# Optimization experiments

Measured on AMD Instinct MI355X. Metric: run time of the kernel, lower is better.

## Reference

```python
import jax, jax.numpy as jnp
import numpy as np

N_NODES = 100000
N_EDGES = 1600000
N_GRAPHS = 128
IN_FEATS = 128
OUT_FEATS = 64


def setup_inputs() -> dict:
    key = jax.random.key(0)
    k1, k2, k3, k4, k5, k6 = jax.random.split(key, 6)
    features = jax.random.normal(k1, (N_NODES, IN_FEATS), jnp.float32)
    src = jax.random.randint(k2, (N_EDGES,), 0, N_NODES, dtype=jnp.int32)
    dst = jax.random.randint(k3, (N_EDGES,), 0, N_NODES, dtype=jnp.int32)
    graph_ids = jnp.sort(jax.random.randint(k4, (N_NODES,), 0, N_GRAPHS, dtype=jnp.int32))
    # Xavier-uniform init as in DGL GraphConv
    lim1 = float(np.sqrt(6.0 / (IN_FEATS + IN_FEATS)))
    lim2 = float(np.sqrt(6.0 / (IN_FEATS + OUT_FEATS)))
    W1 = jax.random.uniform(k5, (IN_FEATS, IN_FEATS), jnp.float32, -lim1, lim1)
    W2 = jax.random.uniform(k6, (IN_FEATS, OUT_FEATS), jnp.float32, -lim2, lim2)
    b1 = jnp.zeros((IN_FEATS,), jnp.float32)
    b2 = jnp.zeros((OUT_FEATS,), jnp.float32)
    return {"features": features, "W1": W1, "b1": b1, "W2": W2, "b2": b2,
            "src": src, "dst": dst, "graph_ids": graph_ids, "num_graphs": N_GRAPHS}


def _graph_conv(x, W, b, src, dst, n_nodes):
    # DGL GraphConv, norm='both': D_dst^{-1/2} A D_src^{-1/2} X W + b
    ones = jnp.ones(src.shape, x.dtype)
    deg_out = jax.ops.segment_sum(ones, src, num_segments=n_nodes)
    deg_in = jax.ops.segment_sum(ones, dst, num_segments=n_nodes)
    norm_src = jax.lax.rsqrt(jnp.maximum(deg_out, 1.0))  # [N]
    norm_dst = jax.lax.rsqrt(jnp.maximum(deg_in, 1.0))   # [N]
    h = (x * norm_src[:, None]) @ W                       # dense transform first
    agg = jax.ops.segment_sum(h[src], dst, num_segments=n_nodes)  # spmm-style scatter-add
    return agg * norm_dst[:, None] + b


def reference(features, W1, b1, W2, b2, src, dst, graph_ids, num_graphs):
    n = features.shape[0]
    h = jax.nn.relu(_graph_conv(features, W1, b1, src, dst, n))
    h = jax.nn.relu(_graph_conv(h, W2, b2, src, dst, n))
    # dgl.mean_nodes: per-graph mean over nodes
    sums = jax.ops.segment_sum(h, graph_ids, num_segments=num_graphs)
    counts = jax.ops.segment_sum(jnp.ones((n, 1), h.dtype), graph_ids, num_segments=num_graphs)
    return sums / jnp.maximum(counts, 1.0)
```

## Files before the change

### kernel.cpp

```cpp
#include <hip/hip_runtime.h>
#include <hip/hip_bf16.h>


#define NPP_SHIFT 9
#define NPP 512
#define MAXP 256
#define NB 512
#define CAPP 10240

typedef __attribute__((ext_vector_type(8))) short frag8;
typedef __attribute__((ext_vector_type(4))) float f32x4;
typedef __attribute__((ext_vector_type(2))) float v2f;

__launch_bounds__(256)
__global__ void buildAC(const int* __restrict__ src, const int* __restrict__ dst,
                        int E, int P, int* __restrict__ cur,
                        int* __restrict__ ebuf_src, int2* __restrict__ ebuf_dst,
                        const int* __restrict__ gids, int N, int G,
                        int* __restrict__ gcnt) {
    __shared__ int hs[MAXP], hd[MAXP], bs1[MAXP], bs2[MAXP], hg[MAXP];
    int tid = threadIdx.x;
    for (int i = tid; i < MAXP; i += 256) { hs[i] = 0; hd[i] = 0; hg[i] = 0; }
    __syncthreads();
    int per_block = (E + NB - 1) / NB;
    int e0 = blockIdx.x * per_block;
    int e1 = min(e0 + per_block, E);
    for (int e = e0 + tid; e < e1; e += 256) {
        atomicAdd(&hs[src[e] >> NPP_SHIFT], 1);
        atomicAdd(&hd[dst[e] >> NPP_SHIFT], 1);
    }
    int npb = (N + NB - 1) / NB;
    int n0 = blockIdx.x * npb;
    int n1 = min(n0 + npb, N);
    for (int i = n0 + tid; i < n1; i += 256) atomicAdd(&hg[gids[i]], 1);
    __syncthreads();
    for (int p = tid; p < P; p += 256) {
        int c1 = hs[p];
        bs1[p] = c1 ? atomicAdd(&cur[p], c1) : 0;
        int c2 = hd[p];
        bs2[p] = c2 ? atomicAdd(&cur[P + p], c2) : 0;
        hs[p] = 0;
        hd[p] = 0;
    }
    for (int i = tid; i < G; i += 256)
        if (hg[i]) atomicAdd(&gcnt[i], hg[i]);
    __syncthreads();
    for (int e = e0 + tid; e < e1; e += 256) {
        int s = src[e];
        int d = dst[e];
        int p1 = s >> NPP_SHIFT;
        int p2 = d >> NPP_SHIFT;
        int l1 = atomicAdd(&hs[p1], 1);
        ebuf_src[(size_t)p1 * CAPP + bs1[p1] + l1] = s;
        int l2 = atomicAdd(&hd[p2], 1);
        ebuf_dst[(size_t)p2 * CAPP + bs2[p2] + l2] = make_int2(d, s);
    }
}

__launch_bounds__(512)
__global__ void passD3(const int* __restrict__ ebuf_src, const int2* __restrict__ ebuf_dst,
                       const int* __restrict__ cur, float* __restrict__ norm_src,
                       int* __restrict__ row_start, int* __restrict__ csr_src,
                       int N, int E, int P) {
    __shared__ int hs[NPP], hd[NPP], sc[NPP];
    int tid = threadIdx.x;
    int p = blockIdx.x;
    sc[tid] = (tid < P) ? cur[P + tid] : 0;
    __syncthreads();
    for (int off = 1; off < 512; off <<= 1) {
        int t = (tid >= off) ? sc[tid - off] : 0;
        __syncthreads();
        sc[tid] += t;
        __syncthreads();
    }
    int gbase = (p > 0) ? sc[p - 1] : 0;
    __syncthreads();
    int node_lo = p << NPP_SHIFT;
    int nl = min(NPP, N - node_lo);
    hs[tid] = 0;
    hd[tid] = 0;
    __syncthreads();
    int nsrc = cur[p];
    size_t base_s = (size_t)p * CAPP;
    for (int i = tid; i < nsrc; i += 512)
        atomicAdd(&hs[ebuf_src[base_s + i] - node_lo], 1);
    int ndst = cur[P + p];
    size_t base_d = (size_t)p * CAPP;
    for (int i = tid; i < ndst; i += 512)
        atomicAdd(&hd[ebuf_dst[base_d + i].x - node_lo], 1);
    __syncthreads();
    if (tid < nl) norm_src[node_lo + tid] = rsqrtf((float)max(hs[tid], 1));
    int myh = hd[tid];
    sc[tid] = myh;
    __syncthreads();
    for (int off = 1; off < 512; off <<= 1) {
        int t = (tid >= off) ? sc[tid - off] : 0;
        __syncthreads();
        sc[tid] += t;
        __syncthreads();
    }
    int row0 = gbase + sc[tid] - myh;
    if (tid < nl) row_start[node_lo + tid] = row0;
    if (p == P - 1 && tid == 0) row_start[N] = E;
    __syncthreads();
    hd[tid] = row0;
    __syncthreads();
    for (int i = tid; i < ndst; i += 512) {
        int2 r = ebuf_dst[base_d + i];
        int pos = atomicAdd(&hd[r.x - node_lo], 1);
        csr_src[pos] = r.y;
    }
}

template <int COLS, bool BF16IN, bool PERM, bool FP8OUT>
__launch_bounds__(256)
__global__ void gemm_mfma(const void* __restrict__ xin, const float* __restrict__ w,
                          const float* __restrict__ norm,
                          void* __restrict__ out, int n) {
    constexpr int NT = COLS / 16;
    __shared__ short wlds[4 * NT * 64 * 8];
    const int tid = threadIdx.x;
    for (int i = tid; i < 128 * COLS / 4; i += 256) {
        int k = (i * 4) / COLS;
        int n0 = (i * 4) % COLS;
        float4 wv;
        if constexpr (PERM) {
            int ksrc = 64 * ((k >> 2) & 1) + 16 * (k & 3) + (k >> 3);
            wv = *reinterpret_cast<const float4*>(w + (size_t)ksrc * COLS + n0);
        } else {
            wv = reinterpret_cast<const float4*>(w)[i];
        }
        int c = k >> 5, q = (k >> 3) & 3, j = k & 7;
        float vals[4] = {wv.x, wv.y, wv.z, wv.w};
#pragma unroll
        for (int u = 0; u < 4; ++u) {
            int nn = n0 + u;
            int t = nn >> 4;
            int ln = (q << 4) | (nn & 15);
            union { __hip_bfloat16 b; short s; } cv;
            cv.b = __float2bfloat16(vals[u]);
            wlds[(((c * NT + t) << 6) | ln) * 8 + j] = cv.s;
        }
    }
    __syncthreads();

    const int lane = tid & 63;
    const int wid = tid >> 6;
    const int m = lane & 15;
    const int q = lane >> 4;
    const int ntiles = (n + 15) >> 4;
    const frag8* wfr = reinterpret_cast<const frag8*>(wlds);

    for (int wt = blockIdx.x * 4 + wid; wt < ntiles; wt += gridDim.x * 4) {
        const int row = (wt << 4) + m;
        frag8 af[4];
        if (row < n) {
            if constexpr (BF16IN) {
                const frag8* xp = reinterpret_cast<const frag8*>(
                    (const __hip_bfloat16*)xin + (size_t)row * 128);
#pragma unroll
                for (int c = 0; c < 4; ++c) af[c] = xp[c * 4 + q];
            } else {
                const float* xp = (const float*)xin + (size_t)row * 128;
                float nm = norm[row];
#pragma unroll
                for (int c = 0; c < 4; ++c) {
                    int base = c * 32 + q * 8;
                    float4 v0 = *reinterpret_cast<const float4*>(xp + base);
                    float4 v1 = *reinterpret_cast<const float4*>(xp + base + 4);
                    union { frag8 f; short s[8]; } a;
                    union { __hip_bfloat16 b; short s; } cv;
                    cv.b = __float2bfloat16(v0.x * nm); a.s[0] = cv.s;
                    cv.b = __float2bfloat16(v0.y * nm); a.s[1] = cv.s;
                    cv.b = __float2bfloat16(v0.z * nm); a.s[2] = cv.s;
                    cv.b = __float2bfloat16(v0.w * nm); a.s[3] = cv.s;
                    cv.b = __float2bfloat16(v1.x * nm); a.s[4] = cv.s;
                    cv.b = __float2bfloat16(v1.y * nm); a.s[5] = cv.s;
                    cv.b = __float2bfloat16(v1.z * nm); a.s[6] = cv.s;
                    cv.b = __float2bfloat16(v1.w * nm); a.s[7] = cv.s;
                    af[c] = a.f;
                }
            }
        } else {
#pragma unroll
            for (int c = 0; c < 4; ++c) af[c] = frag8{0, 0, 0, 0, 0, 0, 0, 0};
        }
        f32x4 acc[NT] = {};
#pragma unroll
        for (int c = 0; c < 4; ++c)
#pragma unroll
            for (int t = 0; t < NT; ++t)
                acc[t] = __builtin_amdgcn_mfma_f32_16x16x32_bf16(
                    af[c], wfr[(c * NT + t) * 64 + lane], acc[t], 0, 0, 0);
#pragma unroll
        for (int r = 0; r < 4; ++r) {
            int grow = (wt << 4) + q * 4 + r;
            if (grow < n) {
                if constexpr (FP8OUT && COLS == 128) {
                    uint w0 = 0, w1 = 0;
                    w0 = (uint)__builtin_amdgcn_cvt_pk_fp8_f32(acc[0][r], acc[1][r], (int)w0, false);
                    w0 = (uint)__builtin_amdgcn_cvt_pk_fp8_f32(acc[2][r], acc[3][r], (int)w0, true);
                    w1 = (uint)__builtin_amdgcn_cvt_pk_fp8_f32(acc[4][r], acc[5][r], (int)w1, false);
                    w1 = (uint)__builtin_amdgcn_cvt_pk_fp8_f32(acc[6][r], acc[7][r], (int)w1, true);
                    reinterpret_cast<uint2*>(out)[(size_t)grow * 16 + m] = make_uint2(w0, w1);
                } else if constexpr (FP8OUT) {
                    uint w0 = 0;
                    w0 = (uint)__builtin_amdgcn_cvt_pk_fp8_f32(acc[0][r], acc[1][r], (int)w0, false);
                    w0 = (uint)__builtin_amdgcn_cvt_pk_fp8_f32(acc[2][r], acc[3][r], (int)w0, true);
                    reinterpret_cast<uint*>(out)[(size_t)grow * 16 + m] = w0;
                } else {
                    __hip_bfloat16* ob = reinterpret_cast<__hip_bfloat16*>(out);
#pragma unroll
                    for (int t = 0; t < NT; ++t)
                        ob[(size_t)grow * COLS + t * 16 + m] = __float2bfloat16(acc[t][r]);
                }
            }
        }
    }
}

__launch_bounds__(256)
__global__ void spmm1_kernel(const uint2* __restrict__ h1,
                             const int* __restrict__ row_start,
                             const int* __restrict__ csr_src,
                             const float* __restrict__ b1,
                             const float* __restrict__ norm_src,
                             uint4* __restrict__ x2n, int n) {
    int wv = (blockIdx.x * blockDim.x + threadIdx.x) >> 6;
    int lane = threadIdx.x & 63;
    int r0 = wv * 2;
    if (r0 >= n) return;
    int a = lane >> 4;
    int s = lane & 15;
    int e0[2], e1[2];
#pragma unroll
    for (int r = 0; r < 2; ++r) {
        int rr = min(r0 + r, n - 1);
        e0[r] = row_start[rr];
        e1[r] = row_start[rr + 1];
        if (r0 + r >= n) e1[r] = e0[r];
    }
    v2f acc[2][4] = {};
    int nb = max((e1[0] - e0[0] + 15) >> 4, (e1[1] - e0[1] + 15) >> 4);
    for (int b = 0; b < nb; ++b) {
        uint2 v[2][4];
#pragma unroll
        for (int r = 0; r < 2; ++r) {
            int base = e0[r] + b * 16;
            if (base + 16 <= e1[r]) {
#pragma unroll
                for (int j = 0; j < 4; ++j)
                    v[r][j] = h1[(size_t)csr_src[base + 4 * j + a] * 16 + s];
            } else if (base < e1[r]) {
#pragma unroll
                for (int j = 0; j < 4; ++j) {
                    int idx = base + 4 * j + a;
                    int cidx = min(idx, e1[r] - 1);
                    uint2 vv = h1[(size_t)csr_src[cidx] * 16 + s];
                    bool ok = idx < e1[r];
                    v[r][j].x = ok ? vv.x : 0u;
                    v[r][j].y = ok ? vv.y : 0u;
                }
            } else {
#pragma unroll
                for (int j = 0; j < 4; ++j) v[r][j] = make_uint2(0u, 0u);
            }
        }
#pragma unroll
        for (int r = 0; r < 2; ++r)
#pragma unroll
            for (int j = 0; j < 4; ++j) {
                acc[r][0] += __builtin_amdgcn_cvt_pk_f32_fp8((int)v[r][j].x, false);
                acc[r][1] += __builtin_amdgcn_cvt_pk_f32_fp8((int)v[r][j].x, true);
                acc[r][2] += __builtin_amdgcn_cvt_pk_f32_fp8((int)v[r][j].y, false);
                acc[r][3] += __builtin_amdgcn_cvt_pk_f32_fp8((int)v[r][j].y, true);
            }
    }
#pragma unroll
    for (int r = 0; r < 2; ++r)
#pragma unroll
        for (int k = 0; k < 4; ++k) {
            v2f t;
            t[0] = __shfl_xor(acc[r][k][0], 16);
            t[1] = __shfl_xor(acc[r][k][1], 16);
            acc[r][k] += t;
            t[0] = __shfl_xor(acc[r][k][0], 32);
            t[1] = __shfl_xor(acc[r][k][1], 32);
            acc[r][k] += t;
        }
    if (a == 0) {
        float bbl[4] = {b1[s], b1[32 + s], b1[64 + s], b1[96 + s]};
        float bbh[4] = {b1[16 + s], b1[48 + s], b1[80 + s], b1[112 + s]};
#pragma unroll
        for (int r = 0; r < 2; ++r) {
            if (r0 + r < n) {
                float nd = rsqrtf((float)max(e1[r] - e0[r], 1));
                float ns = norm_src[r0 + r];
                uint w[4];
#pragma unroll
                for (int k = 0; k < 4; ++k) {
                    float fl = fmaxf(fmaf(acc[r][k][0], nd, bbl[k]), 0.f) * ns;
                    float fh = fmaxf(fmaf(acc[r][k][1], nd, bbh[k]), 0.f) * ns;
                    union { __hip_bfloat16 b; ushort u; } cl, ch;
                    cl.b = __float2bfloat16(fl);
                    ch.b = __float2bfloat16(fh);
                    w[k] = (uint)cl.u | ((uint)ch.u << 16);
                }
                x2n[(size_t)(r0 + r) * 16 + s] = make_uint4(w[0], w[1], w[2], w[3]);
            }
        }
    }
}

__launch_bounds__(256)
__global__ void spmm2_kernel(const uint* __restrict__ h2,
                             const int* __restrict__ row_start,
                             const int* __restrict__ csr_src,
                             const float* __restrict__ b2,
                             const int* __restrict__ gids,
                             const int* __restrict__ gcnt,
                             float* __restrict__ out, int n) {
    int wv = (blockIdx.x * blockDim.x + threadIdx.x) >> 6;
    int lane = threadIdx.x & 63;
    int wave = threadIdx.x >> 6;
    int r0 = wv * 4;
    int a = lane >> 4;
    int s = lane & 15;
    int e0[4], e1[4], g[4];
    float inv[4];
#pragma unroll
    for (int r = 0; r < 4; ++r) {
        int rr = min(r0 + r, n - 1);
        e0[r] = row_start[rr];
        e1[r] = row_start[rr + 1];
        g[r] = gids[rr];
        if (r0 + r >= n) { e1[r] = e0[r]; g[r] = -1; }
        inv[r] = 1.f / (float)max(gcnt[max(g[r], 0)], 1);
    }
    float acc[4][4] = {};
    int nb = 0;
#pragma unroll
    for (int r = 0; r < 4; ++r) nb = max(nb, (e1[r] - e0[r] + 15) >> 4);
    for (int b = 0; b < nb; ++b) {
        uint u[4][4];
#pragma unroll
        for (int r = 0; r < 4; ++r) {
            int base = e0[r] + b * 16;
            if (base + 16 <= e1[r]) {
#pragma unroll
                for (int j = 0; j < 4; ++j)
                    u[r][j] = h2[(size_t)csr_src[base + 4 * j + a] * 16 + s];
            } else if (base < e1[r]) {
#pragma unroll
                for (int j = 0; j < 4; ++j) {
                    int idx = base + 4 * j + a;
                    int cidx = min(idx, e1[r] - 1);
                    uint vv = h2[(size_t)csr_src[cidx] * 16 + s];
                    u[r][j] = (idx < e1[r]) ? vv : 0u;
                }
            } else {
#pragma unroll
                for (int j = 0; j < 4; ++j) u[r][j] = 0u;
            }
        }
#pragma unroll
        for (int r = 0; r < 4; ++r)
#pragma unroll
            for (int j = 0; j < 4; ++j) {
                v2f lo = __builtin_amdgcn_cvt_pk_f32_fp8((int)u[r][j], false);
                v2f hi = __builtin_amdgcn_cvt_pk_f32_fp8((int)u[r][j], true);
                acc[r][0] += lo[0]; acc[r][1] += lo[1];
                acc[r][2] += hi[0]; acc[r][3] += hi[1];
            }
    }
#pragma unroll
    for (int r = 0; r < 4; ++r)
#pragma unroll
        for (int k = 0; k < 4; ++k) {
            acc[r][k] += __shfl_xor(acc[r][k], 16);
            acc[r][k] += __shfl_xor(acc[r][k], 32);
        }
    float bb0 = b2[s], bb1 = b2[16 + s], bb2v = b2[32 + s], bb3 = b2[48 + s];
    float val[4][4];
#pragma unroll
    for (int r = 0; r < 4; ++r) {
        float nd = rsqrtf((float)max(e1[r] - e0[r], 1));
        bool vld = g[r] >= 0;
        val[r][0] = vld ? fmaxf(fmaf(acc[r][0], nd, bb0), 0.f) * inv[r] : 0.f;
        val[r][1] = vld ? fmaxf(fmaf(acc[r][1], nd, bb1), 0.f) * inv[r] : 0.f;
        val[r][2] = vld ? fmaxf(fmaf(acc[r][2], nd, bb2v), 0.f) * inv[r] : 0.f;
        val[r][3] = vld ? fmaxf(fmaf(acc[r][3], nd, bb3), 0.f) * inv[r] : 0.f;
    }
    __shared__ float sbuf[4][64];
    __shared__ int sg[4];
    bool same = (g[0] == g[1]) && (g[1] == g[2]) && (g[2] == g[3]) && (g[0] >= 0);
    int sgw;
    if (same) {
        if (a == 0) {
            sbuf[wave][s]      = val[0][0] + val[1][0] + val[2][0] + val[3][0];
            sbuf[wave][16 + s] = val[0][1] + val[1][1] + val[2][1] + val[3][1];
            sbuf[wave][32 + s] = val[0][2] + val[1][2] + val[2][2] + val[3][2];
            sbuf[wave][48 + s] = val[0][3] + val[1][3] + val[2][3] + val[3][3];
        }
        sgw = g[0];
    } else {
        if (a == 0) {
#pragma unroll
            for (int r = 0; r < 4; ++r) {
                if (g[r] >= 0) {
                    atomicAdd(&out[(size_t)g[r] * 64 + s], val[r][0]);
                    atomicAdd(&out[(size_t)g[r] * 64 + 16 + s], val[r][1]);
                    atomicAdd(&out[(size_t)g[r] * 64 + 32 + s], val[r][2]);
                    atomicAdd(&out[(size_t)g[r] * 64 + 48 + s], val[r][3]);
                }
            }
            sbuf[wave][s] = 0.f;
            sbuf[wave][16 + s] = 0.f;
            sbuf[wave][32 + s] = 0.f;
            sbuf[wave][48 + s] = 0.f;
        }
        sgw = -1;
    }
    if (lane == 0) sg[wave] = sgw;
    __syncthreads();
    if (wave == 0) {
        int g0 = sg[0], g1 = sg[1], g2 = sg[2], g3 = sg[3];
        if (g0 == g1 && g1 == g2 && g2 == g3 && g0 >= 0) {
            float ssum = sbuf[0][lane] + sbuf[1][lane] + sbuf[2][lane] + sbuf[3][lane];
            atomicAdd(&out[(size_t)g0 * 64 + lane], ssum);
        } else {
#pragma unroll
            for (int w = 0; w < 4; ++w)
                if (sg[w] >= 0)
                    atomicAdd(&out[(size_t)sg[w] * 64 + lane], sbuf[w][lane]);
        }
    }
}

extern "C" void kernel_launch(void* const* d_in, const int* in_sizes, int n_in,
                              void* d_out, int out_size, void* d_ws, size_t ws_size,
                              hipStream_t stream) {
    const float* features = (const float*)d_in[0];
    const float* W1 = (const float*)d_in[1];
    const float* b1 = (const float*)d_in[2];
    const float* W2 = (const float*)d_in[3];
    const float* b2 = (const float*)d_in[4];
    const int* src = (const int*)d_in[5];
    const int* dst = (const int*)d_in[6];
    const int* gids = (const int*)d_in[7];
    const int N = in_sizes[7];
    const int E = in_sizes[5];
    const int G = out_size / 64;
    float* out = (float*)d_out;
    const int P = (N + NPP - 1) >> NPP_SHIFT;

    char* ws = (char*)d_ws;
    size_t off = 0;
    auto alloc = [&](size_t bytes) -> void* {
        void* p = ws + off;
        off = (off + bytes + 255) & ~(size_t)255;
        return p;
    };
    int* zblock = (int*)alloc((size_t)(G + 2 * P) * 4);
    int* gcnt = zblock;
    int* cur = zblock + G;
    int* ebuf_src = (int*)alloc((size_t)P * CAPP * 4);
    int2* ebuf_dst = (int2*)alloc((size_t)P * CAPP * 8);
    float* norm_src = (float*)alloc((size_t)N * 4);
    int* row_start = (int*)alloc((size_t)(N + 1) * 4);
    int* csr_src = (int*)alloc((size_t)E * 4);
    uint* h1 = (uint*)alloc((size_t)N * 128);
    __hip_bfloat16* x2n = (__hip_bfloat16*)alloc((size_t)N * 128 * 2);
    uint* h2 = h1;

    hipMemsetAsync(out, 0, (size_t)out_size * sizeof(float), stream);
    hipMemsetAsync(zblock, 0, (size_t)(G + 2 * P) * 4, stream);

    buildAC<<<NB, 256, 0, stream>>>(src, dst, E, P, cur, ebuf_src, ebuf_dst,
                                    gids, N, G, gcnt);
    passD3<<<P, 512, 0, stream>>>(ebuf_src, ebuf_dst, cur, norm_src, row_start,
                                  csr_src, N, E, P);

    gemm_mfma<128, false, false, true><<<768, 256, 0, stream>>>(features, W1, norm_src,
                                                                (void*)h1, N);
    {
        int waves = (N + 1) / 2;
        int blocks = (waves * 64 + 255) / 256;
        spmm1_kernel<<<blocks, 256, 0, stream>>>((const uint2*)h1, row_start, csr_src, b1,
                                                 norm_src, (uint4*)x2n, N);
    }
    gemm_mfma<64, true, true, true><<<768, 256, 0, stream>>>(x2n, W2, nullptr,
                                                             (void*)h2, N);
    {
        int waves = (N + 3) / 4;
        int blocks = (waves * 64 + 255) / 256;
        spmm2_kernel<<<blocks, 256, 0, stream>>>(h2, row_start, csr_src, b2,
                                                 gids, gcnt, out, N);
    }
}
```

Baseline: 285.0 us.

## Bucket edges via striped global atomics with packed compact edge buffers

```diff
diff --git a/kernel.cpp b/kernel.cpp
--- a/kernel.cpp
+++ b/kernel.cpp
@@ -6,109 +6,113 @@
 #define NPP 512
 #define MAXP 256
 #define NB 512
-#define CAPP 10240
+#define CAPB 1280
 
 typedef __attribute__((ext_vector_type(8))) short frag8;
 typedef __attribute__((ext_vector_type(4))) float f32x4;
 typedef __attribute__((ext_vector_type(2))) float v2f;
 
 __launch_bounds__(256)
-__global__ void buildAC(const int* __restrict__ src, const int* __restrict__ dst,
-                        int E, int P, int* __restrict__ cur,
-                        int* __restrict__ ebuf_src, int2* __restrict__ ebuf_dst,
-                        const int* __restrict__ gids, int N, int G,
-                        int* __restrict__ gcnt) {
-    __shared__ int hs[MAXP], hd[MAXP], bs1[MAXP], bs2[MAXP], hg[MAXP];
+__global__ void buildG(const int* __restrict__ src, const int* __restrict__ dst,
+                       int E, int P, int* __restrict__ cur,
+                       ushort* __restrict__ ebuf_src, uint* __restrict__ ebuf_dst,
+                       const int* __restrict__ gids, int N, int G,
+                       int* __restrict__ gcnt) {
+    __shared__ int hg[MAXP];
     int tid = threadIdx.x;
-    for (int i = tid; i < MAXP; i += 256) { hs[i] = 0; hd[i] = 0; hg[i] = 0; }
-    __syncthreads();
-    int per_block = (E + NB - 1) / NB;
-    int e0 = blockIdx.x * per_block;
-    int e1 = min(e0 + per_block, E);
-    for (int e = e0 + tid; e < e1; e += 256) {
-        atomicAdd(&hs[src[e] >> NPP_SHIFT], 1);
-        atomicAdd(&hd[dst[e] >> NPP_SHIFT], 1);
+    for (int i = tid; i < MAXP; i += 256) hg[i] = 0;
+    __syncthreads();
+    int stripe = blockIdx.x & 7;
+    int gt = blockIdx.x * 256 + tid;
+    int stride = gridDim.x * 256;
+    for (int e = gt; e < E; e += stride) {
+        int s = src[e];
+        int d = dst[e];
+        int p1 = s >> NPP_SHIFT;
+        int p2 = d >> NPP_SHIFT;
+        int pos1 = atomicAdd(&cur[(p1 << 3) | stripe], 1);
+        ebuf_src[(size_t)((p1 << 3) | stripe) * CAPB + pos1] = (ushort)(s & 511);
+        int pos2 = atomicAdd(&cur[P * 8 + ((p2 << 3) | stripe)], 1);
+        ebuf_dst[(size_t)((p2 << 3) | stripe) * CAPB + pos2] =
+            ((uint)(d & 511) << 17) | (uint)s;
     }
     int npb = (N + NB - 1) / NB;
     int n0 = blockIdx.x * npb;
     int n1 = min(n0 + npb, N);
     for (int i = n0 + tid; i < n1; i += 256) atomicAdd(&hg[gids[i]], 1);
     __syncthreads();
-    for (int p = tid; p < P; p += 256) {
-        int c1 = hs[p];
-        bs1[p] = c1 ? atomicAdd(&cur[p], c1) : 0;
-        int c2 = hd[p];
-        bs2[p] = c2 ? atomicAdd(&cur[P + p], c2) : 0;
-        hs[p] = 0;
-        hd[p] = 0;
-    }
     for (int i = tid; i < G; i += 256)
         if (hg[i]) atomicAdd(&gcnt[i], hg[i]);
-    __syncthreads();
-    for (int e = e0 + tid; e < e1; e += 256) {
-        int s = src[e];
-        int d = dst[e];
-        int p1 = s >> NPP_SHIFT;
-        int p2 = d >> NPP_SHIFT;
-        int l1 = atomicAdd(&hs[p1], 1);
-        ebuf_src[(size_t)p1 * CAPP + bs1[p1] + l1] = s;
-        int l2 = atomicAdd(&hd[p2], 1);
-        ebuf_dst[(size_t)p2 * CAPP + bs2[p2] + l2] = make_int2(d, s);
-    }
 }
 
-__launch_bounds__(512)
-__global__ void passD3(const int* __restrict__ ebuf_src, const int2* __restrict__ ebuf_dst,
+__launch_bounds__(1024)
+__global__ void passD4(const ushort* __restrict__ ebuf_src, const uint* __restrict__ ebuf_dst,
                        const int* __restrict__ cur, float* __restrict__ norm_src,
                        int* __restrict__ row_start, int* __restrict__ csr_src,
                        int N, int E, int P) {
     __shared__ int hs[NPP], hd[NPP], sc[NPP];
     int tid = threadIdx.x;
     int p = blockIdx.x;
-    sc[tid] = (tid < P) ? cur[P + tid] : 0;
+    if (tid < NPP) {
+        int tot = 0;
+        if (tid < P) {
+#pragma unroll
+            for (int t = 0; t < 8; ++t) tot += cur[P * 8 + (tid << 3) + t];
+        }
+        sc[tid] = tot;
+    }
     __syncthreads();
     for (int off = 1; off < 512; off <<= 1) {
-        int t = (tid >= off) ? sc[tid - off] : 0;
+        int t = (tid >= off && tid < 512) ? sc[tid - off] : 0;
         __syncthreads();
-        sc[tid] += t;
+        if (tid < 512) sc[tid] += t;
         __syncthreads();
     }
     int gbase = (p > 0) ? sc[p - 1] : 0;
+    __syncthreads();
+    if (tid < NPP) { hs[tid] = 0; hd[tid] = 0; }
+    __syncthreads();
+#pragma unroll
+    for (int t = 0; t < 8; ++t) {
+        int cnt = cur[(p << 3) + t];
+        const ushort* eb = ebuf_src + (size_t)((p << 3) + t) * CAPB;
+        for (int i = tid; i < cnt; i += 1024) atomicAdd(&hs[eb[i]], 1);
+    }
+#pragma unroll
+    for (int t = 0; t < 8; ++t) {
+        int cnt = cur[P * 8 + (p << 3) + t];
+        const uint* eb = ebuf_dst + (size_t)((p << 3) + t) * CAPB;
+        for (int i = tid; i < cnt; i += 1024) atomicAdd(&hd[eb[i] >> 17], 1);
+    }
     __syncthreads();
     int node_lo = p << NPP_SHIFT;
     int nl = min(NPP, N - node_lo);
-    hs[tid] = 0;
-    hd[tid] = 0;
-    __syncthreads();
-    int nsrc = cur[p];
-    size_t base_s = (size_t)p * CAPP;
-    for (int i = tid; i < nsrc; i += 512)
-        atomicAdd(&hs[ebuf_src[base_s + i] - node_lo], 1);
-    int ndst = cur[P + p];
-    size_t base_d = (size_t)p * CAPP;
-    for (int i = tid; i < ndst; i += 512)
-        atomicAdd(&hd[ebuf_dst[base_d + i].x - node_lo], 1);
-    __syncthreads();
     if (tid < nl) norm_src[node_lo + tid] = rsqrtf((float)max(hs[tid], 1));
-    int myh = hd[tid];
-    sc[tid] = myh;
+    int myh = (tid < 512) ? hd[tid] : 0;
+    if (tid < 512) sc[tid] = myh;
     __syncthreads();
     for (int off = 1; off < 512; off <<= 1) {
-        int t = (tid >= off) ? sc[tid - off] : 0;
+        int t = (tid >= off && tid < 512) ? sc[tid - off] : 0;
         __syncthreads();
-        sc[tid] += t;
+        if (tid < 512) sc[tid] += t;
         __syncthreads();
     }
-    int row0 = gbase + sc[tid] - myh;
-    if (tid < nl) row_start[node_lo + tid] = row0;
+    if (tid < 512) {
+        int row0 = gbase + sc[tid] - myh;
+        if (tid < nl) row_start[node_lo + tid] = row0;
+        hd[tid] = row0;
+    }
     if (p == P - 1 && tid == 0) row_start[N] = E;
     __syncthreads();
-    hd[tid] = row0;
-    __syncthreads();
-    for (int i = tid; i < ndst; i += 512) {
-        int2 r = ebuf_dst[base_d + i];
-        int pos = atomicAdd(&hd[r.x - node_lo], 1);
-        csr_src[pos] = r.y;
+#pragma unroll
+    for (int t = 0; t < 8; ++t) {
+        int cnt = cur[P * 8 + (p << 3) + t];
+        const uint* eb = ebuf_dst + (size_t)((p << 3) + t) * CAPB;
+        for (int i = tid; i < cnt; i += 1024) {
+            uint r = eb[i];
+            int pos = atomicAdd(&hd[r >> 17], 1);
+            csr_src[pos] = (int)(r & 0x1FFFFu);
+        }
     }
 }
 
@@ -461,11 +465,11 @@
         off = (off + bytes + 255) & ~(size_t)255;
         return p;
     };
-    int* zblock = (int*)alloc((size_t)(G + 2 * P) * 4);
+    int* zblock = (int*)alloc((size_t)(G + 16 * P) * 4);
     int* gcnt = zblock;
     int* cur = zblock + G;
-    int* ebuf_src = (int*)alloc((size_t)P * CAPP * 4);
-    int2* ebuf_dst = (int2*)alloc((size_t)P * CAPP * 8);
+    ushort* ebuf_src = (ushort*)alloc((size_t)P * 8 * CAPB * 2);
+    uint* ebuf_dst = (uint*)alloc((size_t)P * 8 * CAPB * 4);
     float* norm_src = (float*)alloc((size_t)N * 4);
     int* row_start = (int*)alloc((size_t)(N + 1) * 4);
     int* csr_src = (int*)alloc((size_t)E * 4);
@@ -474,12 +478,12 @@
     uint* h2 = h1;
 
     hipMemsetAsync(out, 0, (size_t)out_size * sizeof(float), stream);
-    hipMemsetAsync(zblock, 0, (size_t)(G + 2 * P) * 4, stream);
-
-    buildAC<<<NB, 256, 0, stream>>>(src, dst, E, P, cur, ebuf_src, ebuf_dst,
-                                    gids, N, G, gcnt);
-    passD3<<<P, 512, 0, stream>>>(ebuf_src, ebuf_dst, cur, norm_src, row_start,
-                                  csr_src, N, E, P);
+    hipMemsetAsync(zblock, 0, (size_t)(G + 16 * P) * 4, stream);
+
+    buildG<<<NB, 256, 0, stream>>>(src, dst, E, P, cur, ebuf_src, ebuf_dst,
+                                   gids, N, G, gcnt);
+    passD4<<<P, 1024, 0, stream>>>(ebuf_src, ebuf_dst, cur, norm_src, row_start,
+                                   csr_src, N, E, P);
 
     gemm_mfma<128, false, false, true><<<768, 256, 0, stream>>>(features, W1, norm_src,
                                                                 (void*)h1, N);
```

Measured after the change: 556.5 us. 95.3% more time.
